# Kernel tuning notes

Hardware: AMD Instinct MI355X
Metric: run time of the kernel (lower is better)

Reference implementation:

```python
import jax, jax.numpy as jnp
import numpy as np

NUM_STATES = 16
EMBED_DIM = 512
SEQ_LEN = 512
DIRECTED = True


def setup_inputs() -> dict:
    key = jax.random.key(0)
    k1, k2, k3, k4 = jax.random.split(key, 4)
    # nn.Parameter inits: pos_initial ~ normal, pos_transition ~ orthogonal
    pos_initial = jax.random.normal(k1, (NUM_STATES, 1), dtype=jnp.float32)
    a = jax.random.normal(k2, (NUM_STATES, NUM_STATES), dtype=jnp.float32)
    q, r = jnp.linalg.qr(a)
    pos_transition = q * jnp.sign(jnp.diag(r))[None, :]  # orthogonal init
    # nn.Linear(num_states, embed_dim): W [embed_dim, num_states], bias [embed_dim]
    lim = 1.0 / np.sqrt(NUM_STATES)
    W = jax.random.uniform(k3, (EMBED_DIM, NUM_STATES), minval=-lim, maxval=lim, dtype=jnp.float32)
    b = jax.random.uniform(k4, (EMBED_DIM,), minval=-lim, maxval=lim, dtype=jnp.float32)
    return {
        "pos_initial": pos_initial,
        "pos_transition": pos_transition,
        "W": W,
        "b": b,
        "sentence_len": SEQ_LEN,
    }


def reference(pos_initial, pos_transition, W, b, sentence_len):
    n = int(sentence_len)
    k = pos_initial.shape[0]  # num_states
    ones = jnp.ones(n - 1, dtype=pos_transition.dtype)
    if DIRECTED:
        adj = jnp.diag(ones, 1)  # superdiagonal shift matrix [n, n]
    else:
        adj = jnp.diag(ones, -1) + jnp.diag(ones, 1)
    # (torch code reshapes the square adj to the same shape: a no-op)
    # kron(adj, T): [n*k, n*k]
    kron_prod = jnp.einsum('ab,cd->acbd', adj, pos_transition).reshape(n * k, n * k)
    B = jnp.eye(n * k, dtype=pos_transition.dtype) - kron_prod
    # vec_init: pos_initial column repeated per position -> [n*k]
    vec_init = jnp.tile(pos_initial[:, 0], n)
    encs = jnp.linalg.solve(B, vec_init)  # [n*k]
    stacked = encs.reshape(n, k)          # row i = states of position i
    pe = stacked @ W.T + b                # [n, embed_dim]
    return pe
```

## Files before the change

kernel.cpp:

```cpp
#include <hip/hip_runtime.h>

#define K 16
#define KP 17
#define MAXN 512

__global__ __launch_bounds__(256) void pe_fused(
    const float* __restrict__ pos_initial,
    const float* __restrict__ pos_transition,
    const float* __restrict__ W,
    const float* __restrict__ bias,
    float* __restrict__ out, int n, int E)
{
    __shared__ float sPow[2][K][KP];
    __shared__ float sP[MAXN][K];

    const int tid = threadIdx.x;
    const int r8 = tid >> 4, c8 = tid & 15;

    if (tid < K * K) sPow[0][r8][c8] = pos_transition[tid];
    if (tid < K)     sP[0][tid] = pos_initial[tid];
    __syncthreads();

    int cur = 0;
    for (int s = 1; s < n; s <<= 1) {
        const float (*Tm)[KP] = sPow[cur];

        float sq = 0.f;
        #pragma unroll
        for (int k2 = 0; k2 < K; ++k2) sq += Tm[r8][k2] * Tm[k2][c8];

        const int jmax = (s < n - s) ? s : (n - s);
        for (int e = tid; e < jmax * K; e += 256) {
            const int j = e >> 4, r = e & 15;
            float acc = sP[s - 1][r];
            #pragma unroll
            for (int c = 0; c < K; ++c) acc += Tm[r][c] * sP[j][c];
            sP[j + s][r] = acc;
        }

        sPow[cur ^ 1][r8][c8] = sq;
        cur ^= 1;
        __syncthreads();
    }

    const int i = blockIdx.x;
    const int m1 = n - 1 - i;
    float srow[K];
    #pragma unroll
    for (int r = 0; r < K; ++r) srow[r] = sP[m1][r];

    for (int e = tid; e < E; e += 256) {
        const float4* w4 = reinterpret_cast<const float4*>(W + e * K);
        float4 w0 = w4[0], w1 = w4[1], w2 = w4[2], w3 = w4[3];
        float acc = bias[e];
        acc += w0.x * srow[0]  + w0.y * srow[1]  + w0.z * srow[2]  + w0.w * srow[3];
        acc += w1.x * srow[4]  + w1.y * srow[5]  + w1.z * srow[6]  + w1.w * srow[7];
        acc += w2.x * srow[8]  + w2.y * srow[9]  + w2.z * srow[10] + w2.w * srow[11];
        acc += w3.x * srow[12] + w3.y * srow[13] + w3.z * srow[14] + w3.w * srow[15];
        out[i * E + e] = acc;
    }
}

extern "C" void kernel_launch(void* const* d_in, const int* in_sizes, int n_in,
                              void* d_out, int out_size, void* d_ws, size_t ws_size,
                              hipStream_t stream) {
    const float* pos_initial    = (const float*)d_in[0];
    const float* pos_transition = (const float*)d_in[1];
    const float* W              = (const float*)d_in[2];
    const float* bias           = (const float*)d_in[3];
    const int E = in_sizes[3];
    const int n = out_size / E;

    pe_fused<<<n, 256, 0, stream>>>(pos_initial, pos_transition, W, bias,
                                    (float*)d_out, n, E);
}
```

Before: 70.35 us.

## Vectorize doubling recurrence with register-held matrix rows and halve block count

Each thread now keeps four rows of the current transition power in float4 registers and computes four outputs per position with vectorized LDS reads. A transposed copy of the power matrix lets the squaring use float4 dot products, and the final unneeded squaring is skipped. The grid is halved so each block runs the redundant doubling prefix once and then writes two output rows, cutting duplicated recurrence work across blocks at the cost of fewer blocks in flight and higher register pressure.

```diff
diff --git a/kernel.cpp b/kernel.cpp
--- a/kernel.cpp
+++ b/kernel.cpp
@@ -1,63 +1,95 @@
 #include <hip/hip_runtime.h>
 
 #define K 16
-#define KP 17
+#define RP 20
 #define MAXN 512
+
+static __device__ __forceinline__ float dot4(float4 a, float4 b) {
+    return a.x * b.x + a.y * b.y + a.z * b.z + a.w * b.w;
+}
 
 __global__ __launch_bounds__(256) void pe_fused(
     const float* __restrict__ pos_initial,
     const float* __restrict__ pos_transition,
-    const float* __restrict__ W,
+    const float* __restrict__ Wm,
     const float* __restrict__ bias,
-    float* __restrict__ out, int n, int E)
+    float* __restrict__ out, int n, int E, int nb)
 {
-    __shared__ float sPow[2][K][KP];
-    __shared__ float sP[MAXN][K];
+    __shared__ float sA [2][K][RP];
+    __shared__ float sAT[2][K][RP];
+    __shared__ float sP [MAXN][RP];
 
     const int tid = threadIdx.x;
     const int r8 = tid >> 4, c8 = tid & 15;
 
-    if (tid < K * K) sPow[0][r8][c8] = pos_transition[tid];
-    if (tid < K)     sP[0][tid] = pos_initial[tid];
+    {
+        float t = pos_transition[r8 * K + c8];
+        sA [0][r8][c8] = t;
+        sAT[0][c8][r8] = t;
+    }
+    if (tid < K) sP[0][tid] = pos_initial[tid];
     __syncthreads();
 
     int cur = 0;
     for (int s = 1; s < n; s <<= 1) {
-        const float (*Tm)[KP] = sPow[cur];
-
+        const bool do_sq = (2 * s) < n;
         float sq = 0.f;
-        #pragma unroll
-        for (int k2 = 0; k2 < K; ++k2) sq += Tm[r8][k2] * Tm[k2][c8];
+        if (do_sq) {
+            const float4* ar = (const float4*)&sA [cur][r8][0];
+            const float4* ac = (const float4*)&sAT[cur][c8][0];
+            sq = dot4(ar[0], ac[0]) + dot4(ar[1], ac[1])
+               + dot4(ar[2], ac[2]) + dot4(ar[3], ac[3]);
+        }
 
         const int jmax = (s < n - s) ? s : (n - s);
-        for (int e = tid; e < jmax * K; e += 256) {
-            const int j = e >> 4, r = e & 15;
-            float acc = sP[s - 1][r];
+        const int w = tid >> 6, lane = tid & 63;
+        int rg, j0, jstep; bool part;
+        if (jmax <= 16) { rg = lane >> 4; j0 = lane & 15; jstep = 16; part = (w == 0); }
+        else            { rg = w;         j0 = lane;      jstep = 64; part = true;    }
+        if (part && j0 < jmax) {
+            float4 tm[16];
             #pragma unroll
-            for (int c = 0; c < K; ++c) acc += Tm[r][c] * sP[j][c];
-            sP[j + s][r] = acc;
+            for (int rr = 0; rr < 4; ++rr) {
+                const float4* arow = (const float4*)&sA[cur][4 * rg + rr][0];
+                #pragma unroll
+                for (int q = 0; q < 4; ++q) tm[rr * 4 + q] = arow[q];
+            }
+            const float4 b0 = ((const float4*)&sP[s - 1][0])[rg];
+            for (int j = j0; j < jmax; j += jstep) {
+                const float4* pj = (const float4*)&sP[j][0];
+                const float4 p0 = pj[0], p1 = pj[1], p2 = pj[2], p3 = pj[3];
+                float4 o;
+                o.x = b0.x + dot4(tm[0], p0) + dot4(tm[1], p1) + dot4(tm[2], p2) + dot4(tm[3], p3);
+                o.y = b0.y + dot4(tm[4], p0) + dot4(tm[5], p1) + dot4(tm[6], p2) + dot4(tm[7], p3);
+                o.z = b0.z + dot4(tm[8], p0) + dot4(tm[9], p1) + dot4(tm[10], p2) + dot4(tm[11], p3);
+                o.w = b0.w + dot4(tm[12], p0) + dot4(tm[13], p1) + dot4(tm[14], p2) + dot4(tm[15], p3);
+                ((float4*)&sP[j + s][0])[rg] = o;
+            }
         }
 
-        sPow[cur ^ 1][r8][c8] = sq;
-        cur ^= 1;
+        if (do_sq) {
+            sA [cur ^ 1][r8][c8] = sq;
+            sAT[cur ^ 1][c8][r8] = sq;
+            cur ^= 1;
+        }
         __syncthreads();
     }
 
-    const int i = blockIdx.x;
-    const int m1 = n - 1 - i;
-    float srow[K];
+    const int b = blockIdx.x;
     #pragma unroll
-    for (int r = 0; r < K; ++r) srow[r] = sP[m1][r];
-
-    for (int e = tid; e < E; e += 256) {
-        const float4* w4 = reinterpret_cast<const float4*>(W + e * K);
-        float4 w0 = w4[0], w1 = w4[1], w2 = w4[2], w3 = w4[3];
-        float acc = bias[e];
-        acc += w0.x * srow[0]  + w0.y * srow[1]  + w0.z * srow[2]  + w0.w * srow[3];
-        acc += w1.x * srow[4]  + w1.y * srow[5]  + w1.z * srow[6]  + w1.w * srow[7];
-        acc += w2.x * srow[8]  + w2.y * srow[9]  + w2.z * srow[10] + w2.w * srow[11];
-        acc += w3.x * srow[12] + w3.y * srow[13] + w3.z * srow[14] + w3.w * srow[15];
-        out[i * E + e] = acc;
+    for (int rep = 0; rep < 2; ++rep) {
+        const int i = b + rep * nb;
+        if (i < n) {
+            const int m1 = n - 1 - i;
+            const float4* pm = (const float4*)&sP[m1][0];
+            const float4 p0 = pm[0], p1 = pm[1], p2 = pm[2], p3 = pm[3];
+            for (int e = tid; e < E; e += 256) {
+                const float4* w4 = (const float4*)(Wm + e * K);
+                float acc = bias[e] + dot4(w4[0], p0) + dot4(w4[1], p1)
+                          + dot4(w4[2], p2) + dot4(w4[3], p3);
+                out[i * E + e] = acc;
+            }
+        }
     }
 }
 
@@ -70,7 +102,8 @@
     const float* bias           = (const float*)d_in[3];
     const int E = in_sizes[3];
     const int n = out_size / E;
+    const int nb = (n + 1) / 2;
 
-    pe_fused<<<n, 256, 0, stream>>>(pos_initial, pos_transition, W, bias,
-                                    (float*)d_out, n, E);
+    pe_fused<<<nb, 256, 0, stream>>>(pos_initial, pos_transition, W, bias,
+                                     (float*)d_out, n, E, nb);
 }
```

New measurement: 68.54 us. 2.6% less time.

## Compute each row's geometric series via binary doubling in a single wavefront

Applied to the files above, without the earlier changes.

Replaces the per-block shared-memory prefix construction of all n partial sums with a per-row binary-lifting scheme. Each one-wave block computes only its own sum of T^j·p, using repeated squaring held in registers and cross-lane shuffles, so no LDS or barriers are needed. The intent is to remove the redundant O(n·K²) shared-memory prefix work that every block repeated, plus its synchronisation. In exchange, each block now runs log(n) serial shuffle-heavy 16x16 matrix squarings, and the output GEMV uses 64 threads instead of 256.

```diff
diff --git a/kernel.cpp b/kernel.cpp
--- a/kernel.cpp
+++ b/kernel.cpp
@@ -1,62 +1,81 @@
 #include <hip/hip_runtime.h>
 
 #define K 16
-#define KP 17
-#define MAXN 512
 
-__global__ __launch_bounds__(256) void pe_fused(
+__global__ __launch_bounds__(64) void pe_onewave(
     const float* __restrict__ pos_initial,
     const float* __restrict__ pos_transition,
-    const float* __restrict__ W,
+    const float* __restrict__ Wm,
     const float* __restrict__ bias,
     float* __restrict__ out, int n, int E)
 {
-    __shared__ float sPow[2][K][KP];
-    __shared__ float sP[MAXN][K];
+    const int lane = threadIdx.x;
+    const int r = lane >> 2;
+    const int g = lane & 3;
 
-    const int tid = threadIdx.x;
-    const int r8 = tid >> 4, c8 = tid & 15;
+    float4 P  = ((const float4*)pos_transition)[lane];
+    float4 sc = ((const float4*)pos_initial)[g];
+    float4 cc = make_float4(0.f, 0.f, 0.f, 0.f);
 
-    if (tid < K * K) sPow[0][r8][c8] = pos_transition[tid];
-    if (tid < K)     sP[0][tid] = pos_initial[tid];
-    __syncthreads();
+    const int i = blockIdx.x;
+    const int m = n - i;
 
-    int cur = 0;
-    for (int s = 1; s < n; s <<= 1) {
-        const float (*Tm)[KP] = sPow[cur];
+    for (int k = 0; k < 31; ++k) {
+        if ((m >> k) & 1) {
+            float part = P.x * cc.x + P.y * cc.y + P.z * cc.z + P.w * cc.w;
+            part += __shfl_xor(part, 1);
+            part += __shfl_xor(part, 2);
+            cc.x = sc.x + __shfl(part, 16 * g);
+            cc.y = sc.y + __shfl(part, 16 * g + 4);
+            cc.z = sc.z + __shfl(part, 16 * g + 8);
+            cc.w = sc.w + __shfl(part, 16 * g + 12);
+        }
+        if ((m >> (k + 1)) == 0) break;
 
-        float sq = 0.f;
-        #pragma unroll
-        for (int k2 = 0; k2 < K; ++k2) sq += Tm[r8][k2] * Tm[k2][c8];
-
-        const int jmax = (s < n - s) ? s : (n - s);
-        for (int e = tid; e < jmax * K; e += 256) {
-            const int j = e >> 4, r = e & 15;
-            float acc = sP[s - 1][r];
-            #pragma unroll
-            for (int c = 0; c < K; ++c) acc += Tm[r][c] * sP[j][c];
-            sP[j + s][r] = acc;
+        {
+            float part = P.x * sc.x + P.y * sc.y + P.z * sc.z + P.w * sc.w;
+            part += __shfl_xor(part, 1);
+            part += __shfl_xor(part, 2);
+            sc.x += __shfl(part, 16 * g);
+            sc.y += __shfl(part, 16 * g + 4);
+            sc.z += __shfl(part, 16 * g + 8);
+            sc.w += __shfl(part, 16 * g + 12);
         }
-
-        sPow[cur ^ 1][r8][c8] = sq;
-        cur ^= 1;
-        __syncthreads();
+        {
+            float4 acc = make_float4(0.f, 0.f, 0.f, 0.f);
+            #pragma unroll 16
+            for (int kk = 0; kk < 16; ++kk) {
+                float a;
+                switch (kk & 3) {
+                    case 0:  a = __shfl(P.x, 4 * r + (kk >> 2)); break;
+                    case 1:  a = __shfl(P.y, 4 * r + (kk >> 2)); break;
+                    case 2:  a = __shfl(P.z, 4 * r + (kk >> 2)); break;
+                    default: a = __shfl(P.w, 4 * r + (kk >> 2)); break;
+                }
+                float bx = __shfl(P.x, 4 * kk + g);
+                float by = __shfl(P.y, 4 * kk + g);
+                float bz = __shfl(P.z, 4 * kk + g);
+                float bw = __shfl(P.w, 4 * kk + g);
+                acc.x += a * bx; acc.y += a * by; acc.z += a * bz; acc.w += a * bw;
+            }
+            P = acc;
+        }
     }
 
-    const int i = blockIdx.x;
-    const int m1 = n - 1 - i;
-    float srow[K];
-    #pragma unroll
-    for (int r = 0; r < K; ++r) srow[r] = sP[m1][r];
+    float4 x0, x1, x2, x3;
+    x0.x = __shfl(cc.x, 0); x0.y = __shfl(cc.y, 0); x0.z = __shfl(cc.z, 0); x0.w = __shfl(cc.w, 0);
+    x1.x = __shfl(cc.x, 1); x1.y = __shfl(cc.y, 1); x1.z = __shfl(cc.z, 1); x1.w = __shfl(cc.w, 1);
+    x2.x = __shfl(cc.x, 2); x2.y = __shfl(cc.y, 2); x2.z = __shfl(cc.z, 2); x2.w = __shfl(cc.w, 2);
+    x3.x = __shfl(cc.x, 3); x3.y = __shfl(cc.y, 3); x3.z = __shfl(cc.z, 3); x3.w = __shfl(cc.w, 3);
 
-    for (int e = tid; e < E; e += 256) {
-        const float4* w4 = reinterpret_cast<const float4*>(W + e * K);
+    for (int e = lane; e < E; e += 64) {
+        const float4* w4 = (const float4*)(Wm + e * K);
         float4 w0 = w4[0], w1 = w4[1], w2 = w4[2], w3 = w4[3];
         float acc = bias[e];
-        acc += w0.x * srow[0]  + w0.y * srow[1]  + w0.z * srow[2]  + w0.w * srow[3];
-        acc += w1.x * srow[4]  + w1.y * srow[5]  + w1.z * srow[6]  + w1.w * srow[7];
-        acc += w2.x * srow[8]  + w2.y * srow[9]  + w2.z * srow[10] + w2.w * srow[11];
-        acc += w3.x * srow[12] + w3.y * srow[13] + w3.z * srow[14] + w3.w * srow[15];
+        acc += w0.x * x0.x + w0.y * x0.y + w0.z * x0.z + w0.w * x0.w;
+        acc += w1.x * x1.x + w1.y * x1.y + w1.z * x1.z + w1.w * x1.w;
+        acc += w2.x * x2.x + w2.y * x2.y + w2.z * x2.z + w2.w * x2.w;
+        acc += w3.x * x3.x + w3.y * x3.y + w3.z * x3.z + w3.w * x3.w;
         out[i * E + e] = acc;
     }
 }
@@ -71,6 +90,6 @@
     const int E = in_sizes[3];
     const int n = out_size / E;
 
-    pe_fused<<<n, 256, 0, stream>>>(pos_initial, pos_transition, W, bias,
-                                    (float*)d_out, n, E);
+    pe_onewave<<<n, 64, 0, stream>>>(pos_initial, pos_transition, W, bias,
+                                     (float*)d_out, n, E);
 }
```

New measurement: 68.88 us. 2.1% less time.
